# Performance work log

Measured on AMD Instinct MI355X. Metric: run time of the kernel, lower is better.

The kernel has to match this reference:

```python
import jax, jax.numpy as jnp
import numpy as np
from functools import partial

B, T, D_IN, H, D_OUT = 64, 2048, 256, 256, 128


def setup_inputs() -> dict:
    key = jax.random.key(0)
    ks = jax.random.split(key, 12)
    w = lambda k, shape: (jax.random.normal(k, shape, jnp.float32) * 0.05)
    inp = {
        "h": jax.random.normal(ks[0], (B, T, D_IN), jnp.float32),
        # linear_h_a: Linear(input_dim, hidden_dim, bias=False)
        "W_h_a": w(ks[1], (H, D_IN)),
        # linear_s_a: Linear(hidden_dim, hidden_dim, bias=True)
        "W_s_a": w(ks[2], (H, H)),
        "b_s_a": w(ks[3], (H,)),
        # linear_a: Linear(2*hidden_dim, 1, bias=False)
        "W_a": w(ks[4], (1, 2 * H)),
        # linear_init_s: Linear(input_dim, hidden_dim, bias=True)
        "W_init": w(ks[5], (H, D_IN)),
        "b_init": w(ks[6], (H,)),
        # GRUCell(output_dim+input_dim, hidden_dim); input is cat((ci, yim)) -> (D_IN + D_OUT)
        "W_ih_g": w(ks[7], (3 * H, D_IN + D_OUT)),
        "W_hh_g": w(ks[8], (3 * H, H)),
        "b_ih_g": jnp.zeros((3 * H,), jnp.float32),
        "b_hh_g": jnp.zeros((3 * H,), jnp.float32),
        # RNNCell(hidden_dim+input_dim, output_dim); input is cat((ci, si)) -> (D_IN + H)
        "W_ih_r": w(ks[9], (D_OUT, D_IN + H)),
        "W_hh_r": w(ks[10], (D_OUT, D_OUT)),
        "b_ih_r": jnp.zeros((D_OUT,), jnp.float32),
        "b_hh_r": jnp.zeros((D_OUT,), jnp.float32),
        "out_len": 64,
    }
    return inp


def _gru_cell(x, hp, W_ih, W_hh, b_ih, b_hh):
    gi = x @ W_ih.T + b_ih
    gh = hp @ W_hh.T + b_hh
    i_r, i_z, i_n = jnp.split(gi, 3, axis=1)
    h_r, h_z, h_n = jnp.split(gh, 3, axis=1)
    r = jax.nn.sigmoid(i_r + h_r)
    z = jax.nn.sigmoid(i_z + h_z)
    n = jnp.tanh(i_n + r * h_n)
    return (1.0 - z) * n + z * hp


def _rnn_cell(x, hp, W_ih, W_hh, b_ih, b_hh):
    return jnp.tanh(x @ W_ih.T + b_ih + hp @ W_hh.T + b_hh)


def _decode(h, W_h_a, W_s_a, b_s_a, W_a, W_init, b_init,
            W_ih_g, W_hh_g, b_ih_g, b_hh_g,
            W_ih_r, W_hh_r, b_ih_r, b_hh_r, out_len):
    # wh = linear_h_a(h): (B, T, H)
    wh = jnp.einsum("btd,hd->bth", h, W_h_a)
    # tanh(cat(wh, sa)) is elementwise, so the concat+linear_a splits exactly:
    # score = tanh(wh) @ W_a[:H] + tanh(sa) @ W_a[H:]
    wa1 = W_a[0, :W_s_a.shape[0]]
    wa2 = W_a[0, W_s_a.shape[0]:]
    twh = jnp.tanh(wh) @ wa1                       # (B, T) precomputed once

    s0 = jnp.tanh(h[:, 0, :] @ W_init.T + b_init)  # initHidden
    y0 = jnp.zeros((h.shape[0], W_ih_r.shape[0]), h.dtype)  # initSeq

    def step(carry, _):
        s, y = carry
        sa = jnp.tanh(s @ W_s_a.T + b_s_a) @ wa2   # (B,)
        a = jax.nn.softmax(twh + sa[:, None], axis=1)      # (B, T)
        ci = jnp.einsum("bt,btd->bd", a, h)                # context (B, D_in)
        si = _gru_cell(jnp.concatenate([ci, y], axis=1), s,
                       W_ih_g, W_hh_g, b_ih_g, b_hh_g)
        yi = jax.nn.softmax(
            _rnn_cell(jnp.concatenate([ci, si], axis=1), y,
                      W_ih_r, W_hh_r, b_ih_r, b_hh_r), axis=1)
        return (si, yi), yi

    _, ys = jax.lax.scan(step, (s0, y0), None, length=out_len)
    return jnp.transpose(ys, (1, 0, 2))  # (B, out_len, D_out)


def reference(h, W_h_a, W_s_a, b_s_a, W_a, W_init, b_init,
              W_ih_g, W_hh_g, b_ih_g, b_hh_g,
              W_ih_r, W_hh_r, b_ih_r, b_hh_r, out_len):
    return _decode(h, W_h_a, W_s_a, b_s_a, W_a, W_init, b_init,
                   W_ih_g, W_hh_g, b_ih_g, b_hh_g,
                   W_ih_r, W_hh_r, b_ih_r, b_hh_r, out_len)
```

## Files before the change

### kernel.cpp

```cpp
#include <hip/hip_runtime.h>
#include <cstdint>

typedef unsigned short ushort_t;
typedef __attribute__((ext_vector_type(8))) short short8;
typedef __attribute__((ext_vector_type(4))) short short4_t;
typedef __attribute__((ext_vector_type(4))) float f4;

#define BB   64
#define TT   2048
#define DD   256
#define DO_  128
#define OL   64

#define O_TWH   0
#define O_RMAX  131072
#define O_RDEN  131136
#define O_CIP   131200
#define O_CI    393344
#define O_GIC   409728
#define O_RIC   458880
#define O_S0    467072
#define O_SG    483456
#define O_LP    516224
#define O_CTR   647296
#define O_RWS   647808
#define O_RWY   680576
#define O_US    696960
#define U_WB    0
#define U_BG    65536

static __device__ __forceinline__ ushort_t f2bf(float f) {
  union { float f; uint32_t u; } v; v.f = f;
  uint32_t u = v.u;
  u += 0x7FFFu + ((u >> 16) & 1u);
  return (ushort_t)(u >> 16);
}
static __device__ __forceinline__ float fast_tanh(float x) {
  float e = __expf(2.f * x);
  return 1.f - 2.f / (e + 1.f);
}
static __device__ __forceinline__ float fast_sigmoid(float x) {
  return 1.f / (1.f + __expf(-x));
}
static __device__ __forceinline__ void llc_store(float* p, float v) {
  __hip_atomic_store(p, v, __ATOMIC_RELAXED, __HIP_MEMORY_SCOPE_AGENT);
}

__global__ __launch_bounds__(256) void k_prep(const float* __restrict__ Wha,
    const float* __restrict__ Whhg, const float* __restrict__ Wihg,
    const float* __restrict__ Wihr, const float* __restrict__ Whhr,
    float* __restrict__ ws, ushort_t* __restrict__ us) {
  int idx = blockIdx.x * 256 + threadIdx.x;
  if (idx < 65536) {
    us[U_WB + idx] = f2bf(Wha[idx]);
    return;
  }
  if (idx < 65536 + 294912) {
    int i = idx - 65536;
    int pos = i & 7;
    int l = (i >> 3) & 63;
    int r = i >> 9;
    int kb = r % 12;
    int r2 = r / 12;
    int n = r2 % 6;
    int blk = r2 / 6;
    int c = n * 16 + (l & 15);
    int g = c >> 5;
    int kl = c & 31;
    int kg = 32 * blk + kl;
    int j = kb * 32 + ((l >> 4) & 3) * 8 + pos;
    int row = g * 256 + kg;
    float v;
    if (j < 256) v = Whhg[row * 256 + j];
    else         v = Wihg[row * 384 + j];
    us[U_BG + i] = f2bf(v);
    return;
  }
  if (idx < 65536 + 294912 + 32768) {
    int i = idx - (65536 + 294912);
    int m = i & 127, kl = (i >> 7) & 31, blk = i >> 12;
    ws[O_RWS + i] = Wihr[m * 512 + 256 + 32 * blk + kl];
  } else {
    int i = idx - (65536 + 294912 + 32768);
    int m = i & 127, jl = (i >> 7) & 15, blk = i >> 11;
    ws[O_RWY + i] = Whhr[m * 128 + 16 * blk + jl];
  }
}

__global__ __launch_bounds__(256) void k_twh(const float* __restrict__ h,
                                             const ushort_t* __restrict__ Wb,
                                             const float* __restrict__ Wa,
                                             float* __restrict__ twh) {
  __shared__ __align__(16) ushort_t alds[64 * 264];
  __shared__ float walds[256];
  const int tid = threadIdx.x;
  const long rowbase = (long)blockIdx.x * 64;
  walds[tid] = Wa[tid];
  for (int it = 0; it < 8; ++it) {
    int q = it * 256 + tid;
    int r = q >> 5;
    int c8 = q & 31;
    const float* src = h + (rowbase + r) * 256 + c8 * 8;
    float4 a = *(const float4*)(src);
    float4 b = *(const float4*)(src + 4);
    union { ushort_t u[8]; short8 v; } t;
    t.u[0]=f2bf(a.x); t.u[1]=f2bf(a.y); t.u[2]=f2bf(a.z); t.u[3]=f2bf(a.w);
    t.u[4]=f2bf(b.x); t.u[5]=f2bf(b.y); t.u[6]=f2bf(b.z); t.u[7]=f2bf(b.w);
    *(short8*)&alds[r * 264 + c8 * 8] = t.v;
  }
  __syncthreads();
  const int l = tid & 63, w = tid >> 6;
  const int cres = l & 15, kg = l >> 4;
  f4 acc[16];
  #pragma unroll
  for (int f = 0; f < 16; ++f) acc[f] = (f4){0.f, 0.f, 0.f, 0.f};
  const int arow = 16 * w + cres;
  #pragma unroll
  for (int ks = 0; ks < 8; ++ks) {
    short8 af = *(const short8*)&alds[arow * 264 + ks * 32 + kg * 8];
    const ushort_t* bp = Wb + ks * 32 + kg * 8 + cres * 256;
    #pragma unroll
    for (int f = 0; f < 16; ++f) {
      short8 bf = *(const short8*)(bp + f * 16 * 256);
      acc[f] = __builtin_amdgcn_mfma_f32_16x16x32_bf16(af, bf, acc[f], 0, 0, 0);
    }
  }
  float t4[4] = {0.f, 0.f, 0.f, 0.f};
  #pragma unroll
  for (int f = 0; f < 16; ++f) {
    float wa = walds[16 * f + cres];
    #pragma unroll
    for (int r = 0; r < 4; ++r) t4[r] += fast_tanh(acc[f][r]) * wa;
  }
  #pragma unroll
  for (int m = 1; m <= 8; m <<= 1) {
    #pragma unroll
    for (int r = 0; r < 4; ++r) t4[r] += __shfl_xor(t4[r], m);
  }
  if (cres == 0) {
    #pragma unroll
    for (int r = 0; r < 4; ++r)
      twh[rowbase + 16 * w + kg * 4 + r] = t4[r];
  }
}

__global__ __launch_bounds__(256) void k_stats(const float* __restrict__ twh,
                                               float* __restrict__ rmax,
                                               float* __restrict__ rden) {
  __shared__ float redm[4], reds[4];
  const int b = blockIdx.x, tid = threadIdx.x;
  float v[8];
  #pragma unroll
  for (int j = 0; j < 8; ++j) v[j] = twh[b * 2048 + tid + j * 256];
  float mx = v[0];
  #pragma unroll
  for (int j = 1; j < 8; ++j) mx = fmaxf(mx, v[j]);
  #pragma unroll
  for (int d = 32; d >= 1; d >>= 1) mx = fmaxf(mx, __shfl_xor(mx, d));
  if ((tid & 63) == 0) redm[tid >> 6] = mx;
  __syncthreads();
  float M = fmaxf(fmaxf(redm[0], redm[1]), fmaxf(redm[2], redm[3]));
  float s = 0.f;
  #pragma unroll
  for (int j = 0; j < 8; ++j) s += __expf(v[j] - M);
  #pragma unroll
  for (int d = 32; d >= 1; d >>= 1) s += __shfl_xor(s, d);
  if ((tid & 63) == 0) reds[tid >> 6] = s;
  __syncthreads();
  if (tid == 0) { rmax[b] = M; rden[b] = reds[0] + reds[1] + reds[2] + reds[3]; }
}

__global__ __launch_bounds__(256) void k_cipart(const float* __restrict__ h,
                                                const float* __restrict__ twh,
                                                const float* __restrict__ rmax,
                                                float* __restrict__ cipart) {
  __shared__ float p[128];
  const int b = blockIdx.x >> 4, ts = blockIdx.x & 15;
  const int tid = threadIdx.x;
  const int t0 = ts * 128;
  if (tid < 128) p[tid] = __expf(twh[b * 2048 + t0 + tid] - rmax[b]);
  __syncthreads();
  float acc = 0.f;
  const float* hp = h + ((long)(b * 2048 + t0)) * 256 + tid;
  #pragma unroll 8
  for (int i = 0; i < 128; ++i) { acc += p[i] * hp[0]; hp += 256; }
  cipart[(b * 16 + ts) * 256 + tid] = acc;
}

__global__ __launch_bounds__(256) void k_cired(const float* __restrict__ cipart,
                                               const float* __restrict__ rden,
                                               float* __restrict__ ci) {
  const int b = blockIdx.x, d = threadIdx.x;
  float a = 0.f;
  #pragma unroll
  for (int ts = 0; ts < 16; ++ts) a += cipart[(b * 16 + ts) * 256 + d];
  ci[b * 256 + d] = a / rden[b];
}

__global__ __launch_bounds__(256) void k_const(const float* __restrict__ h,
    const float* __restrict__ ci,
    const float* __restrict__ Wihg, const float* __restrict__ bihg,
    const float* __restrict__ bhhg,
    const float* __restrict__ Wihr, const float* __restrict__ bihr,
    const float* __restrict__ bhhr,
    const float* __restrict__ Winit, const float* __restrict__ binit,
    float* __restrict__ gic, float* __restrict__ ric, float* __restrict__ s0) {
  __shared__ float cil[256], h0l[256];
  const int b = blockIdx.x, tid = threadIdx.x;
  cil[tid] = ci[b * 256 + tid];
  h0l[tid] = h[(long)b * 2048 * 256 + tid];
  __syncthreads();
  const int k = tid;
  #pragma unroll
  for (int g = 0; g < 3; ++g) {
    float a = bihg[g * 256 + k] + (g < 2 ? bhhg[g * 256 + k] : 0.f);
    const float* wp = Wihg + (long)(g * 256 + k) * 384;
    for (int d = 0; d < 256; d += 4) {
      float4 w4 = *(const float4*)(wp + d);
      a += cil[d] * w4.x + cil[d + 1] * w4.y + cil[d + 2] * w4.z + cil[d + 3] * w4.w;
    }
    gic[b * 768 + g * 256 + k] = a;
  }
  {
    float a = binit[k];
    const float* wp = Winit + (long)k * 256;
    for (int d = 0; d < 256; d += 4) {
      float4 w4 = *(const float4*)(wp + d);
      a += h0l[d] * w4.x + h0l[d + 1] * w4.y + h0l[d + 2] * w4.z + h0l[d + 3] * w4.w;
    }
    s0[b * 256 + k] = fast_tanh(a);
  }
  if (tid < 128) {
    int m = tid;
    float a = bihr[m] + bhhr[m];
    const float* wp = Wihr + (long)m * 512;
    for (int d = 0; d < 256; d += 4) {
      float4 w4 = *(const float4*)(wp + d);
      a += cil[d] * w4.x + cil[d + 1] * w4.y + cil[d + 2] * w4.z + cil[d + 3] * w4.w;
    }
    ric[b * 128 + m] = a;
  }
}

__global__ __launch_bounds__(512) void k_loop(
    const float* __restrict__ gic, const float* __restrict__ ric,
    const float* __restrict__ s0w, const float* __restrict__ bhhg,
    const ushort_t* __restrict__ BG, const float* __restrict__ RWSg,
    const float* __restrict__ RWYg,
    float* __restrict__ sg, float* __restrict__ lp,
    unsigned int* __restrict__ ctr,
    float* __restrict__ out) {
  __shared__ __align__(16) ushort_t Bl[36864];
  __shared__ __align__(16) ushort_t Al[6144];
  __shared__ float RWSl[32][128];
  __shared__ float RWYl[16][128];
  __shared__ float gsum[8][128];
  __shared__ float sslice[8][32];
  __shared__ float ybuf[8][128];
  __shared__ float ricl[8][128];
  __shared__ float gicl[8][3][32];
  __shared__ float bnl[32];
  const int tid = threadIdx.x;
  const int grp = blockIdx.x & 7;
  const int blk = blockIdx.x >> 3;
  const int b0 = grp * 8;

  {
    const short8* src = (const short8*)(BG + (long)blk * 36864);
    short8* dst = (short8*)Bl;
    for (int i = tid; i < 4608; i += 512) dst[i] = src[i];
  }
  for (int i = tid; i < 4096; i += 512) ((float*)RWSl)[i] = RWSg[blk * 4096 + i];
  for (int i = tid; i < 2048; i += 512) ((float*)RWYl)[i] = RWYg[blk * 2048 + i];
  for (int i = tid; i < 1024; i += 512) ((float*)ricl)[i] = ric[b0 * 128 + i];
  for (int i = tid; i < 768; i += 512) {
    int bb = i / 96, rem = i % 96, g = rem >> 5, kl = rem & 31;
    gicl[bb][g][kl] = gic[(b0 + bb) * 768 + g * 256 + blk * 32 + kl];
  }
  if (tid < 32) bnl[tid] = bhhg[512 + blk * 32 + tid];
  if (tid < 256) {
    int bb = tid >> 5, kl = tid & 31;
    sslice[bb][kl] = s0w[(b0 + bb) * 256 + blk * 32 + kl];
  }
  for (int i = tid; i < 1024; i += 512) ((float*)ybuf)[i] = 0.f;
  for (int i = tid; i < 3072; i += 512) {
    int kb = i >> 8, rem = i & 255, kg = rem >> 6, row = 8 + ((rem >> 3) & 7), pos = rem & 7;
    Al[((kb * 4 + kg) * 16 + row) * 8 + pos] = 0;
  }
  __syncthreads();

  for (int it = 0; it <= OL; ++it) {
    const int par = it & 1;
    const int bb1 = tid >> 6, ml = tid & 63;
    f4 sgv;
    if (it > 0) {
      const float* aL = lp + (((long)((par * 8 + grp) * 8 + bb1)) << 10) + ml;
      const float* a2 = sg + par * 16384 + (b0 + bb1) * 256 + ml * 4;
      float r0,r1,r2,r3,r4,r5,r6,r7,r8,r9,r10,r11,r12,r13,r14,r15;
      asm volatile(
        "global_load_dword %0, %17, off sc0 sc1\n\t"
        "global_load_dword %1, %17, off offset:512 sc0 sc1\n\t"
        "global_load_dword %2, %17, off offset:1024 sc0 sc1\n\t"
        "global_load_dword %3, %17, off offset:1536 sc0 sc1\n\t"
        "global_load_dword %4, %17, off offset:2048 sc0 sc1\n\t"
        "global_load_dword %5, %17, off offset:2560 sc0 sc1\n\t"
        "global_load_dword %6, %17, off offset:3072 sc0 sc1\n\t"
        "global_load_dword %7, %17, off offset:3584 sc0 sc1\n\t"
        "global_load_dword %8, %17, off offset:256 sc0 sc1\n\t"
        "global_load_dword %9, %17, off offset:768 sc0 sc1\n\t"
        "global_load_dword %10, %17, off offset:1280 sc0 sc1\n\t"
        "global_load_dword %11, %17, off offset:1792 sc0 sc1\n\t"
        "global_load_dword %12, %17, off offset:2304 sc0 sc1\n\t"
        "global_load_dword %13, %17, off offset:2816 sc0 sc1\n\t"
        "global_load_dword %14, %17, off offset:3328 sc0 sc1\n\t"
        "global_load_dword %15, %17, off offset:3840 sc0 sc1\n\t"
        "global_load_dwordx4 %16, %18, off sc0 sc1\n\t"
        "s_waitcnt vmcnt(0)"
        : "=&v"(r0), "=&v"(r1), "=&v"(r2), "=&v"(r3),
          "=&v"(r4), "=&v"(r5), "=&v"(r6), "=&v"(r7),
          "=&v"(r8), "=&v"(r9), "=&v"(r10), "=&v"(r11),
          "=&v"(r12), "=&v"(r13), "=&v"(r14), "=&v"(r15),
          "=&v"(sgv)
        : "v"(aL), "v"(a2)
        : "memory");
      float L0 = ricl[bb1][ml]      + ((r0+r1)+(r2+r3)) + ((r4+r5)+(r6+r7));
      float L1 = ricl[bb1][ml + 64] + ((r8+r9)+(r10+r11)) + ((r12+r13)+(r14+r15));
      L0 = fast_tanh(L0); L1 = fast_tanh(L1);
      float e0 = __expf(L0), e1 = __expf(L1);
      float s = e0 + e1;
      #pragma unroll
      for (int d = 32; d >= 1; d >>= 1) s += __shfl_xor(s, d);
      float y0 = e0 / s, y1 = e1 / s;
      ybuf[bb1][ml] = y0; ybuf[bb1][ml + 64] = y1;
      if (bb1 == blk) {
        float* op = out + ((long)(b0 + blk) * OL + (it - 1)) * DO_;
        op[ml] = y0; op[ml + 64] = y1;
      }
    } else {
      sgv = *(const f4*)(s0w + (b0 + bb1) * 256 + ml * 4);
    }
    if (it == OL) break;
    __syncthreads();
    {
      const int j4 = ml * 4;
      int kb = j4 >> 5, kg = (j4 >> 3) & 3, pos = j4 & 7;
      short4_t h4;
      h4[0] = (short)f2bf(sgv[0]); h4[1] = (short)f2bf(sgv[1]);
      h4[2] = (short)f2bf(sgv[2]); h4[3] = (short)f2bf(sgv[3]);
      *(short4_t*)&Al[((kb * 4 + kg) * 16 + bb1) * 8 + pos] = h4;
    }
    if (tid < 256) {
      const int bb = tid >> 5, jl4 = (tid & 31) * 4;
      const int j = 256 + jl4;
      int kb = j >> 5, kg = (j >> 3) & 3, pos = j & 7;
      short4_t h4;
      h4[0] = (short)f2bf(ybuf[bb][jl4]);     h4[1] = (short)f2bf(ybuf[bb][jl4 + 1]);
      h4[2] = (short)f2bf(ybuf[bb][jl4 + 2]); h4[3] = (short)f2bf(ybuf[bb][jl4 + 3]);
      *(short4_t*)&Al[((kb * 4 + kg) * 16 + bb) * 8 + pos] = h4;
    }
    __syncthreads();
    if (tid < 128) {
      const int w = tid >> 6, l = tid & 63;
      f4 a0 = (f4){0,0,0,0}, a1 = (f4){0,0,0,0}, a2v = (f4){0,0,0,0};
      f4 m1 = (f4){0,0,0,0}, m2 = (f4){0,0,0,0};
      const short8* Ap = (const short8*)Al + l;
      const short8* Bp = (const short8*)Bl + (w * 3) * 768 + l;
      #pragma unroll
      for (int kb = 0; kb < 12; ++kb) {
        short8 af = Ap[kb * 64];
        a0 = __builtin_amdgcn_mfma_f32_16x16x32_bf16(af, Bp[kb * 64], a0, 0, 0, 0);
        a1 = __builtin_amdgcn_mfma_f32_16x16x32_bf16(af, Bp[768 + kb * 64], a1, 0, 0, 0);
        a2v = __builtin_amdgcn_mfma_f32_16x16x32_bf16(af, Bp[1536 + kb * 64], a2v, 0, 0, 0);
        if (kb == 7) { m1 = a1; m2 = a2v; }
      }
      if (l < 32) {
        const int bbase = (l >> 4) * 4, c = l & 15;
        if (w == 0) {
          #pragma unroll
          for (int r = 0; r < 4; ++r) {
            gsum[bbase + r][c]      = a0[r];
            gsum[bbase + r][16 + c] = a1[r];
            gsum[bbase + r][32 + c] = a2v[r];
          }
        } else {
          #pragma unroll
          for (int r = 0; r < 4; ++r) {
            gsum[bbase + r][48 + c] = a0[r];
            gsum[bbase + r][64 + c]      = m1[r];
            gsum[bbase + r][96 + c]      = a1[r] - m1[r];
            gsum[bbase + r][64 + 16 + c] = m2[r];
            gsum[bbase + r][96 + 16 + c] = a2v[r] - m2[r];
          }
        }
      }
    }
    __syncthreads();
    if (tid < 256) {
      const int bb = tid >> 5, kl = tid & 31;
      float sold = sslice[bb][kl];
      float R   = fast_sigmoid(gsum[bb][kl]      + gicl[bb][0][kl]);
      float Z   = fast_sigmoid(gsum[bb][32 + kl] + gicl[bb][1][kl]);
      float hn  = gsum[bb][64 + kl] + bnl[kl];
      float in_ = gsum[bb][96 + kl] + gicl[bb][2][kl];
      float N = fast_tanh(in_ + R * hn);
      float sn = (1.f - Z) * N + Z * sold;
      sslice[bb][kl] = sn;
      llc_store(sg + (par ^ 1) * 16384 + (b0 + bb) * 256 + blk * 32 + kl, sn);
    }
    __syncthreads();
    {
      const int m = tid & 127, q = tid >> 7;
      const int ba = 2 * q, bbv = 2 * q + 1;
      float acc0 = 0.f, acc1 = 0.f;
      #pragma unroll 8
      for (int kl = 0; kl < 32; ++kl) {
        float w = RWSl[kl][m];
        acc0 += w * sslice[ba][kl];
        acc1 += w * sslice[bbv][kl];
      }
      #pragma unroll 8
      for (int jl = 0; jl < 16; ++jl) {
        float w = RWYl[jl][m];
        acc0 += w * ybuf[ba][16 * blk + jl];
        acc1 += w * ybuf[bbv][16 * blk + jl];
      }
      float* dst = lp + (((long)((par ^ 1) * 8 + grp) * 8) << 10) + blk * 128 + m;
      llc_store(dst + (ba  << 10), acc0);
      llc_store(dst + (bbv << 10), acc1);
    }
    __syncthreads();
    if (tid == 0) {
      unsigned int* c = ctr + grp * 64 + it;
      __hip_atomic_fetch_add(c, 1u, __ATOMIC_RELAXED, __HIP_MEMORY_SCOPE_AGENT);
      while (__hip_atomic_load(c, __ATOMIC_RELAXED, __HIP_MEMORY_SCOPE_AGENT) < 8u) {
        __builtin_amdgcn_s_sleep(2);
      }
    }
    __syncthreads();
  }
}

extern "C" void kernel_launch(void* const* d_in, const int* in_sizes, int n_in,
                              void* d_out, int out_size, void* d_ws, size_t ws_size,
                              hipStream_t stream) {
  const float* h     = (const float*)d_in[0];
  const float* Wha   = (const float*)d_in[1];
  const float* Wa    = (const float*)d_in[4];
  const float* Winit = (const float*)d_in[5];
  const float* binit = (const float*)d_in[6];
  const float* Wihg  = (const float*)d_in[7];
  const float* Whhg  = (const float*)d_in[8];
  const float* bihg  = (const float*)d_in[9];
  const float* bhhg  = (const float*)d_in[10];
  const float* Wihr  = (const float*)d_in[11];
  const float* Whhr  = (const float*)d_in[12];
  const float* bihr  = (const float*)d_in[13];
  const float* bhhr  = (const float*)d_in[14];
  float* ws  = (float*)d_ws;
  float* out = (float*)d_out;
  ushort_t* us = (ushort_t*)(ws + O_US);

  hipMemsetAsync((char*)d_ws + (size_t)O_CTR * 4, 0, 512 * 4, stream);

  k_prep<<<dim3(1600), dim3(256), 0, stream>>>(Wha, Whhg, Wihg, Wihr, Whhr, ws, us);
  k_twh<<<dim3(2048), dim3(256), 0, stream>>>(h, us + U_WB, Wa, ws + O_TWH);
  k_stats<<<dim3(64), dim3(256), 0, stream>>>(ws + O_TWH, ws + O_RMAX, ws + O_RDEN);
  k_cipart<<<dim3(1024), dim3(256), 0, stream>>>(h, ws + O_TWH, ws + O_RMAX, ws + O_CIP);
  k_cired<<<dim3(64), dim3(256), 0, stream>>>(ws + O_CIP, ws + O_RDEN, ws + O_CI);
  k_const<<<dim3(64), dim3(256), 0, stream>>>(h, ws + O_CI, Wihg, bihg, bhhg,
                                              Wihr, bihr, bhhr, Winit, binit,
                                              ws + O_GIC, ws + O_RIC, ws + O_S0);
  k_loop<<<dim3(64), dim3(512), 0, stream>>>(ws + O_GIC, ws + O_RIC, ws + O_S0, bhhg,
                                             us + U_BG, ws + O_RWS, ws + O_RWY,
                                             ws + O_SG, ws + O_LP,
                                             (unsigned int*)(ws + O_CTR),
                                             out);
}
```

Baseline: 472.7 us.

## Replace per-step counter barrier with epoch tags in data low bits

```diff
diff --git a/kernel.cpp b/kernel.cpp
--- a/kernel.cpp
+++ b/kernel.cpp
@@ -35,6 +35,9 @@
   u += 0x7FFFu + ((u >> 16) & 1u);
   return (ushort_t)(u >> 16);
 }
+static __device__ __forceinline__ uint32_t fbits(float f) {
+  union { float f; uint32_t u; } v; v.f = f; return v.u;
+}
 static __device__ __forceinline__ float fast_tanh(float x) {
   float e = __expf(2.f * x);
   return 1.f - 2.f / (e + 1.f);
@@ -42,8 +45,10 @@
 static __device__ __forceinline__ float fast_sigmoid(float x) {
   return 1.f / (1.f + __expf(-x));
 }
-static __device__ __forceinline__ void llc_store(float* p, float v) {
-  __hip_atomic_store(p, v, __ATOMIC_RELAXED, __HIP_MEMORY_SCOPE_AGENT);
+static __device__ __forceinline__ void llc_store_tag(float* p, float v, uint32_t tag) {
+  union { float f; uint32_t u; } x; x.f = v;
+  x.u = (x.u & ~3u) | tag;
+  __hip_atomic_store((uint32_t*)p, x.u, __ATOMIC_RELAXED, __HIP_MEMORY_SCOPE_AGENT);
 }
 
 __global__ __launch_bounds__(256) void k_prep(const float* __restrict__ Wha,
@@ -248,7 +253,6 @@
     const ushort_t* __restrict__ BG, const float* __restrict__ RWSg,
     const float* __restrict__ RWYg,
     float* __restrict__ sg, float* __restrict__ lp,
-    unsigned int* __restrict__ ctr,
     float* __restrict__ out) {
   __shared__ __align__(16) ushort_t Bl[36864];
   __shared__ __align__(16) ushort_t Al[6144];
@@ -294,35 +298,50 @@
     const int bb1 = tid >> 6, ml = tid & 63;
     f4 sgv;
     if (it > 0) {
+      const uint32_t texp = (((uint32_t)it) >> 1) & 3u;
       const float* aL = lp + (((long)((par * 8 + grp) * 8 + bb1)) << 10) + ml;
       const float* a2 = sg + par * 16384 + (b0 + bb1) * 256 + ml * 4;
       float r0,r1,r2,r3,r4,r5,r6,r7,r8,r9,r10,r11,r12,r13,r14,r15;
-      asm volatile(
-        "global_load_dword %0, %17, off sc0 sc1\n\t"
-        "global_load_dword %1, %17, off offset:512 sc0 sc1\n\t"
-        "global_load_dword %2, %17, off offset:1024 sc0 sc1\n\t"
-        "global_load_dword %3, %17, off offset:1536 sc0 sc1\n\t"
-        "global_load_dword %4, %17, off offset:2048 sc0 sc1\n\t"
-        "global_load_dword %5, %17, off offset:2560 sc0 sc1\n\t"
-        "global_load_dword %6, %17, off offset:3072 sc0 sc1\n\t"
-        "global_load_dword %7, %17, off offset:3584 sc0 sc1\n\t"
-        "global_load_dword %8, %17, off offset:256 sc0 sc1\n\t"
-        "global_load_dword %9, %17, off offset:768 sc0 sc1\n\t"
-        "global_load_dword %10, %17, off offset:1280 sc0 sc1\n\t"
-        "global_load_dword %11, %17, off offset:1792 sc0 sc1\n\t"
-        "global_load_dword %12, %17, off offset:2304 sc0 sc1\n\t"
-        "global_load_dword %13, %17, off offset:2816 sc0 sc1\n\t"
-        "global_load_dword %14, %17, off offset:3328 sc0 sc1\n\t"
-        "global_load_dword %15, %17, off offset:3840 sc0 sc1\n\t"
-        "global_load_dwordx4 %16, %18, off sc0 sc1\n\t"
-        "s_waitcnt vmcnt(0)"
-        : "=&v"(r0), "=&v"(r1), "=&v"(r2), "=&v"(r3),
-          "=&v"(r4), "=&v"(r5), "=&v"(r6), "=&v"(r7),
-          "=&v"(r8), "=&v"(r9), "=&v"(r10), "=&v"(r11),
-          "=&v"(r12), "=&v"(r13), "=&v"(r14), "=&v"(r15),
-          "=&v"(sgv)
-        : "v"(aL), "v"(a2)
-        : "memory");
+      while (true) {
+        asm volatile(
+          "global_load_dword %0, %17, off sc0 sc1\n\t"
+          "global_load_dword %1, %17, off offset:512 sc0 sc1\n\t"
+          "global_load_dword %2, %17, off offset:1024 sc0 sc1\n\t"
+          "global_load_dword %3, %17, off offset:1536 sc0 sc1\n\t"
+          "global_load_dword %4, %17, off offset:2048 sc0 sc1\n\t"
+          "global_load_dword %5, %17, off offset:2560 sc0 sc1\n\t"
+          "global_load_dword %6, %17, off offset:3072 sc0 sc1\n\t"
+          "global_load_dword %7, %17, off offset:3584 sc0 sc1\n\t"
+          "global_load_dword %8, %17, off offset:256 sc0 sc1\n\t"
+          "global_load_dword %9, %17, off offset:768 sc0 sc1\n\t"
+          "global_load_dword %10, %17, off offset:1280 sc0 sc1\n\t"
+          "global_load_dword %11, %17, off offset:1792 sc0 sc1\n\t"
+          "global_load_dword %12, %17, off offset:2304 sc0 sc1\n\t"
+          "global_load_dword %13, %17, off offset:2816 sc0 sc1\n\t"
+          "global_load_dword %14, %17, off offset:3328 sc0 sc1\n\t"
+          "global_load_dword %15, %17, off offset:3840 sc0 sc1\n\t"
+          "global_load_dwordx4 %16, %18, off sc0 sc1\n\t"
+          "s_waitcnt vmcnt(0)"
+          : "=&v"(r0), "=&v"(r1), "=&v"(r2), "=&v"(r3),
+            "=&v"(r4), "=&v"(r5), "=&v"(r6), "=&v"(r7),
+            "=&v"(r8), "=&v"(r9), "=&v"(r10), "=&v"(r11),
+            "=&v"(r12), "=&v"(r13), "=&v"(r14), "=&v"(r15),
+            "=&v"(sgv)
+          : "v"(aL), "v"(a2)
+          : "memory");
+        uint32_t bad = (fbits(r0) ^ texp) | (fbits(r1) ^ texp) |
+                       (fbits(r2) ^ texp) | (fbits(r3) ^ texp) |
+                       (fbits(r4) ^ texp) | (fbits(r5) ^ texp) |
+                       (fbits(r6) ^ texp) | (fbits(r7) ^ texp) |
+                       (fbits(r8) ^ texp) | (fbits(r9) ^ texp) |
+                       (fbits(r10) ^ texp) | (fbits(r11) ^ texp) |
+                       (fbits(r12) ^ texp) | (fbits(r13) ^ texp) |
+                       (fbits(r14) ^ texp) | (fbits(r15) ^ texp) |
+                       (fbits(sgv[0]) ^ texp) | (fbits(sgv[1]) ^ texp) |
+                       (fbits(sgv[2]) ^ texp) | (fbits(sgv[3]) ^ texp);
+        if ((bad & 3u) == 0u) break;
+        __builtin_amdgcn_s_sleep(1);
+      }
       float L0 = ricl[bb1][ml]      + ((r0+r1)+(r2+r3)) + ((r4+r5)+(r6+r7));
       float L1 = ricl[bb1][ml + 64] + ((r8+r9)+(r10+r11)) + ((r12+r13)+(r14+r15));
       L0 = fast_tanh(L0); L1 = fast_tanh(L1);
@@ -395,20 +414,24 @@
       }
     }
     __syncthreads();
-    if (tid < 256) {
-      const int bb = tid >> 5, kl = tid & 31;
-      float sold = sslice[bb][kl];
-      float R   = fast_sigmoid(gsum[bb][kl]      + gicl[bb][0][kl]);
-      float Z   = fast_sigmoid(gsum[bb][32 + kl] + gicl[bb][1][kl]);
-      float hn  = gsum[bb][64 + kl] + bnl[kl];
-      float in_ = gsum[bb][96 + kl] + gicl[bb][2][kl];
-      float N = fast_tanh(in_ + R * hn);
-      float sn = (1.f - Z) * N + Z * sold;
-      sslice[bb][kl] = sn;
-      llc_store(sg + (par ^ 1) * 16384 + (b0 + bb) * 256 + blk * 32 + kl, sn);
+    {
+      const uint32_t tprod = (((uint32_t)it + 1u) >> 1) & 3u;
+      if (tid < 256) {
+        const int bb = tid >> 5, kl = tid & 31;
+        float sold = sslice[bb][kl];
+        float R   = fast_sigmoid(gsum[bb][kl]      + gicl[bb][0][kl]);
+        float Z   = fast_sigmoid(gsum[bb][32 + kl] + gicl[bb][1][kl]);
+        float hn  = gsum[bb][64 + kl] + bnl[kl];
+        float in_ = gsum[bb][96 + kl] + gicl[bb][2][kl];
+        float N = fast_tanh(in_ + R * hn);
+        float sn = (1.f - Z) * N + Z * sold;
+        sslice[bb][kl] = sn;
+        llc_store_tag(sg + (par ^ 1) * 16384 + (b0 + bb) * 256 + blk * 32 + kl, sn, tprod);
+      }
     }
     __syncthreads();
     {
+      const uint32_t tprod = (((uint32_t)it + 1u) >> 1) & 3u;
       const int m = tid & 127, q = tid >> 7;
       const int ba = 2 * q, bbv = 2 * q + 1;
       float acc0 = 0.f, acc1 = 0.f;
@@ -425,16 +448,8 @@
         acc1 += w * ybuf[bbv][16 * blk + jl];
       }
       float* dst = lp + (((long)((par ^ 1) * 8 + grp) * 8) << 10) + blk * 128 + m;
-      llc_store(dst + (ba  << 10), acc0);
-      llc_store(dst + (bbv << 10), acc1);
-    }
-    __syncthreads();
-    if (tid == 0) {
-      unsigned int* c = ctr + grp * 64 + it;
-      __hip_atomic_fetch_add(c, 1u, __ATOMIC_RELAXED, __HIP_MEMORY_SCOPE_AGENT);
-      while (__hip_atomic_load(c, __ATOMIC_RELAXED, __HIP_MEMORY_SCOPE_AGENT) < 8u) {
-        __builtin_amdgcn_s_sleep(2);
-      }
+      llc_store_tag(dst + (ba  << 10), acc0, tprod);
+      llc_store_tag(dst + (bbv << 10), acc1, tprod);
     }
     __syncthreads();
   }
@@ -460,7 +475,10 @@
   float* out = (float*)d_out;
   ushort_t* us = (ushort_t*)(ws + O_US);
 
-  hipMemsetAsync((char*)d_ws + (size_t)O_CTR * 4, 0, 512 * 4, stream);
+  hipMemsetAsync((char*)d_ws + (size_t)O_SG * 4,             0x00, 16384 * 4, stream);
+  hipMemsetAsync((char*)d_ws + (size_t)(O_SG + 16384) * 4,   0xFF, 16384 * 4, stream);
+  hipMemsetAsync((char*)d_ws + (size_t)O_LP * 4,             0x00, 65536 * 4, stream);
+  hipMemsetAsync((char*)d_ws + (size_t)(O_LP + 65536) * 4,   0xFF, 65536 * 4, stream);
 
   k_prep<<<dim3(1600), dim3(256), 0, stream>>>(Wha, Whhg, Wihg, Wihr, Whhr, ws, us);
   k_twh<<<dim3(2048), dim3(256), 0, stream>>>(h, us + U_WB, Wa, ws + O_TWH);
@@ -473,6 +491,5 @@
   k_loop<<<dim3(64), dim3(512), 0, stream>>>(ws + O_GIC, ws + O_RIC, ws + O_S0, bhhg,
                                              us + U_BG, ws + O_RWS, ws + O_RWY,
                                              ws + O_SG, ws + O_LP,
-                                             (unsigned int*)(ws + O_CTR),
                                              out);
 }
```

Measured after the change: 452.9 us. 1.04x faster.
